# Performance work log

Hardware: AMD Instinct MI355X
Metric: run time of the kernel (lower is better)

Reference implementation:

```python
import jax, jax.numpy as jnp
import numpy as np
import math

EMBED_DIM = 2048
NUM_HEADS = 32
NUM_KV_HEADS = 8
HEAD_DIM = EMBED_DIM // NUM_HEADS  # 64
N_REP = NUM_HEADS // NUM_KV_HEADS  # 4
BATCH = 2
SEQ = 2048


def _rope_tables(seq_len, head_dim):
    # standard RoPE tables matching rotate_half convention (frequencies tiled twice)
    inv_freq = 1.0 / (10000.0 ** (np.arange(0, head_dim, 2, dtype=np.float32) / head_dim))
    t = np.arange(seq_len, dtype=np.float32)
    freqs = np.outer(t, inv_freq)                      # (seq, head_dim/2)
    emb = np.concatenate([freqs, freqs], axis=-1)      # (seq, head_dim)
    return jnp.asarray(np.cos(emb)), jnp.asarray(np.sin(emb))


def setup_inputs() -> dict:
    key = jax.random.key(0)
    ks = jax.random.split(key, 6)
    scale = 1.0 / math.sqrt(EMBED_DIM)
    x = jax.random.normal(ks[0], (BATCH, SEQ, EMBED_DIM), dtype=jnp.float32)
    wq = jax.random.normal(ks[1], (EMBED_DIM, EMBED_DIM), dtype=jnp.float32) * scale
    wk = jax.random.normal(ks[2], (NUM_KV_HEADS * HEAD_DIM, EMBED_DIM), dtype=jnp.float32) * scale
    wv = jax.random.normal(ks[3], (NUM_KV_HEADS * HEAD_DIM, EMBED_DIM), dtype=jnp.float32) * scale
    wo = jax.random.normal(ks[4], (EMBED_DIM, EMBED_DIM), dtype=jnp.float32) * scale
    freqs_cos, freqs_sin = _rope_tables(SEQ, HEAD_DIM)
    return {"x": x, "freqs_cos": freqs_cos, "freqs_sin": freqs_sin,
            "wq": wq, "wk": wk, "wv": wv, "wo": wo}


def _rotate_half(t):
    h = t.shape[-1] // 2
    return jnp.concatenate([-t[..., h:], t[..., :h]], axis=-1)


def reference(x, freqs_cos, freqs_sin, wq, wk, wv, wo):
    b, s, _ = x.shape
    # QKV projections (Linear with weight (out,in): y = x @ W^T)
    xq = (x @ wq.T).reshape(b, s, NUM_HEADS, HEAD_DIM).transpose(0, 2, 1, 3)     # (b,H,s,d)
    xk = (x @ wk.T).reshape(b, s, NUM_KV_HEADS, HEAD_DIM).transpose(0, 2, 1, 3)  # (b,Hkv,s,d)
    xv = (x @ wv.T).reshape(b, s, NUM_KV_HEADS, HEAD_DIM).transpose(0, 2, 1, 3)
    # RoPE: cos/sin (s,d) broadcast over (b,h,s,d)
    xq = xq * freqs_cos + _rotate_half(xq) * freqs_sin
    xk = xk * freqs_cos + _rotate_half(xk) * freqs_sin
    # GQA: repeat_interleave kv heads to match q heads
    xk = jnp.repeat(xk, N_REP, axis=1)  # (b,H,s,d)
    xv = jnp.repeat(xv, N_REP, axis=1)
    scores = jnp.einsum('bhqd,bhkd->bhqk', xq, xk) / math.sqrt(HEAD_DIM)
    causal = jnp.tril(jnp.ones((s, s), dtype=bool))
    scores = jnp.where(causal, scores, jnp.float32(-1e30))
    attn = jax.nn.softmax(scores, axis=-1)
    out = jnp.einsum('bhqk,bhkd->bhqd', attn, xv)        # (b,H,s,d)
    out = out.transpose(0, 2, 1, 3).reshape(b, s, EMBED_DIM)
    return out @ wo.T
```

## Files before the change

### kernel.cpp

```cpp
#include <hip/hip_runtime.h>

#define BATCH 2
#define SEQ 2048
#define EMBED 2048
#define NHEADS 32
#define NKV 8
#define HDIM 64
#define QKV_LD 3072
#define LOG2E 1.44269504088896f

typedef __attribute__((ext_vector_type(8))) short short8;
typedef __attribute__((ext_vector_type(4))) float f32x4;

__device__ inline float hw_exp2(float x) { return __builtin_amdgcn_exp2f(x); }

__device__ inline ushort f2bf(float f) {
  union { float f; unsigned u; } v{f};
  unsigned r = v.u + 0x7FFF + ((v.u >> 16) & 1);
  return (ushort)(r >> 16);
}
__device__ inline float bf2f(ushort u) {
  union { unsigned u; float f; } v{((unsigned)u) << 16};
  return v.f;
}
__device__ inline unsigned fbits(float f) {
  union { float f; unsigned u; } v{f};
  return v.u;
}

__device__ inline void gload16(const ushort* g, ushort* l) {
  __builtin_amdgcn_global_load_lds(
      (const __attribute__((address_space(1))) unsigned*)g,
      (__attribute__((address_space(3))) unsigned*)l, 16, 0, 0);
}

#define PHASE_BAR()                          \
  do {                                       \
    __builtin_amdgcn_sched_barrier(0);       \
    __builtin_amdgcn_s_barrier();            \
    __builtin_amdgcn_sched_barrier(0);       \
  } while (0)

__global__ __launch_bounds__(256) void cvt_all(const float* __restrict__ x,
                                               const float* __restrict__ wq,
                                               const float* __restrict__ wk,
                                               const float* __restrict__ wv,
                                               const float* __restrict__ wo,
                                               ushort* __restrict__ xb,
                                               ushort* __restrict__ wqkv,
                                               ushort* __restrict__ wob) {
  size_t e = (size_t)(blockIdx.x * blockDim.x + threadIdx.x) * 8;
  const float* src;
  ushort* dst;
  if (e < 8388608u) { src = x + e; dst = xb + e; }
  else if (e < 12582912u) { size_t o = e - 8388608u; src = wq + o; dst = wqkv + o; }
  else if (e < 13631488u) { size_t o = e - 12582912u; src = wk + o; dst = wqkv + 4194304u + o; }
  else if (e < 14680064u) { size_t o = e - 13631488u; src = wv + o; dst = wqkv + 5242880u + o; }
  else { size_t o = e - 14680064u; src = wo + o; dst = wob + o; }
  float4 v0 = ((const float4*)src)[0];
  float4 v1 = ((const float4*)src)[1];
  union { uint4 v; ushort u[8]; } pk;
  pk.u[0] = f2bf(v0.x); pk.u[1] = f2bf(v0.y); pk.u[2] = f2bf(v0.z); pk.u[3] = f2bf(v0.w);
  pk.u[4] = f2bf(v1.x); pk.u[5] = f2bf(v1.y); pk.u[6] = f2bf(v1.z); pk.u[7] = f2bf(v1.w);
  *(uint4*)dst = pk.v;
}

template <int BN, int MODE, typename OutT>
__global__ __launch_bounds__(512) void gemm8p(const ushort* __restrict__ Ag,
                                              const ushort* __restrict__ Bg,
                                              OutT* __restrict__ C,
                                              const float* __restrict__ fc,
                                              const float* __restrict__ fs,
                                              int M, int N, int K) {
  constexpr int NF = BN / 64;
  __shared__ ushort As[2][2][256][32];
  __shared__ ushort Bs[2][2][BN][32];
  const int tid = threadIdx.x;
  const int lane = tid & 63, wave = tid >> 6;
  const int quad = lane >> 4, l16 = lane & 15;
  const int wm = wave >> 2, wn = wave & 3;
  const int m0 = blockIdx.y * 256, n0 = blockIdx.x * BN;
  const int NT = K >> 6;

  auto stA = [&](int Tn, int h) {
    const int r0 = h * 128 + wave * 16;
    const int lrow = r0 + (lane >> 2);
    const int sw = ((lane & 3) ^ ((lrow >> 1) & 3)) * 8;
    const ushort* g = Ag + (size_t)(m0 + lrow) * K + Tn * 64 + sw;
    gload16(g, &As[Tn & 1][0][r0][0]);
    gload16(g + 32, &As[Tn & 1][1][r0][0]);
  };
  auto stB = [&](int Tn, int h) {
    const int r0 = h * 128 + wave * 16;
    const int lrow = r0 + (lane >> 2);
    const int sw = ((lane & 3) ^ ((lrow >> 1) & 3)) * 8;
    const ushort* g = Bg + (size_t)(n0 + lrow) * K + Tn * 64 + sw;
    gload16(g, &Bs[Tn & 1][0][r0][0]);
    gload16(g + 32, &Bs[Tn & 1][1][r0][0]);
  };

  f32x4 acc[8][NF] = {};

  stA(0, 0); stA(0, 1);
  stB(0, 0);
  if constexpr (BN == 256) stB(0, 1);

  for (int T = 0; T < NT; ++T) {
    const int bf = T & 1;
    asm volatile("s_waitcnt vmcnt(0)" ::: "memory");
    PHASE_BAR();

    short8 bfr[NF][2];
#pragma unroll
    for (int nf = 0; nf < NF; nf++) {
      const int row = wn * (16 * NF) + nf * 16 + l16;
      const int ch = (quad ^ ((row >> 1) & 3)) * 8;
#pragma unroll
      for (int kk = 0; kk < 2; kk++)
        bfr[nf][kk] = *(short8*)&Bs[bf][kk][row][ch];
    }

#pragma unroll
    for (int q = 0; q < 4; q++) {
      short8 afr[2][2];
#pragma unroll
      for (int mq = 0; mq < 2; mq++) {
        const int row = wm * 128 + (2 * q + mq) * 16 + l16;
        const int ch = (quad ^ ((row >> 1) & 3)) * 8;
#pragma unroll
        for (int kk = 0; kk < 2; kk++)
          afr[mq][kk] = *(short8*)&As[bf][kk][row][ch];
      }

      if (T + 1 < NT) {
        if (q == 0) stA(T + 1, 0);
        else if (q == 1) stA(T + 1, 1);
        else if (q == 2) stB(T + 1, 0);
        else if constexpr (BN == 256) stB(T + 1, 1);
      }

      __builtin_amdgcn_s_setprio(1);
#pragma unroll
      for (int mq = 0; mq < 2; mq++)
#pragma unroll
        for (int nf = 0; nf < NF; nf++)
#pragma unroll
          for (int kk = 0; kk < 2; kk++)
            acc[2 * q + mq][nf] = __builtin_amdgcn_mfma_f32_16x16x32_bf16(
                afr[mq][kk], bfr[nf][kk], acc[2 * q + mq][nf], 0, 0, 0);
      __builtin_amdgcn_s_setprio(0);
      PHASE_BAR();
    }
  }

  if constexpr (MODE == 1) {
    if (n0 < 2560) {
      const float scale = (n0 < 2048) ? 0.125f * LOG2E : 1.0f;
      const int d0 = l16, d1 = l16 + 32;
      const int e0 = l16 + 16, e1 = l16 + 48;
#pragma unroll
      for (int mf = 0; mf < 8; mf++) {
#pragma unroll
        for (int r = 0; r < 4; r++) {
          size_t rg = (size_t)(m0 + wm * 128 + mf * 16 + quad * 4 + r);
          int s = (int)(rg & (SEQ - 1));
          const float* cb = fc + s * HDIM;
          const float* sb = fs + s * HDIM;
          float x0 = acc[mf][0][r], x2 = acc[mf][2][r];
          float y1 = acc[mf][1][r], y3 = acc[mf][3][r];
          float o0 = (x0 * cb[d0] - x2 * sb[d0]) * scale;
          float o2 = (x2 * cb[d1] + x0 * sb[d1]) * scale;
          float o1 = (y1 * cb[e0] - y3 * sb[e0]) * scale;
          float o3 = (y3 * cb[e1] + y1 * sb[e1]) * scale;
          ushort* Cr = (ushort*)C + rg * N + n0 + wn * 64 + l16;
          Cr[0]  = f2bf(o0);
          Cr[16] = f2bf(o1);
          Cr[32] = f2bf(o2);
          Cr[48] = f2bf(o3);
        }
      }
      return;
    }
  }
#pragma unroll
  for (int mf = 0; mf < 8; mf++) {
#pragma unroll
    for (int r = 0; r < 4; r++) {
      size_t rg = (size_t)(m0 + wm * 128 + mf * 16 + quad * 4 + r);
#pragma unroll
      for (int nf = 0; nf < NF; nf++) {
        int cg = n0 + wn * (16 * NF) + nf * 16 + l16;
        if constexpr (sizeof(OutT) == 2)
          C[rg * N + cg] = f2bf(acc[mf][nf][r]);
        else
          C[rg * N + cg] = acc[mf][nf][r];
      }
    }
  }
}

__global__ __launch_bounds__(256, 4) void attn_mfma(const ushort* __restrict__ QKV,
                                                    ushort* __restrict__ O) {
  __shared__ ushort Ks[64][72];
  __shared__ ushort Vt[64][72];
  __shared__ ushort Pw[4][16][72];
  const int tid = threadIdx.x;
  const int lane = tid & 63, wave = tid >> 6;
  const int quad = lane >> 4, l16 = lane & 15;

  const int bid = blockIdx.x;
  const int qq = bid >> 8;
  const int j4 = (bid >> 6) & 3;
  const int bh = bid & 63;
  const int qblk = (qq >> 1) * 8 + ((qq & 1) ? 7 - j4 : j4);

  const int b = bh >> 5, h = bh & 31, kh = h >> 2;
  const int ntiles = 2 * qblk + 2;
  const int wrow = qblk * 128 + wave * 32;

  short8 qf[2][2];
#pragma unroll
  for (int f = 0; f < 2; f++)
#pragma unroll
    for (int c = 0; c < 2; c++)
      qf[f][c] = *(const short8*)(QKV +
          (size_t)(b * SEQ + wrow + f * 16 + l16) * QKV_LD +
          h * HDIM + c * 32 + quad * 8);

  f32x4 o[2][4] = {};
  float m[2] = {-INFINITY, -INFINITY}, l[2] = {0.f, 0.f};

  const ushort* Kbase = QKV + (size_t)b * SEQ * QKV_LD + 2048 + kh * HDIM;
  const ushort* Vbase = Kbase + 512;
  const int kp = tid & 31, dg = tid >> 5;

  for (int t = 0; t < ntiles; t++) {
    const int k0 = t * 64;
    __syncthreads();
    {
      const float4* kpp = (const float4*)(Kbase + (size_t)(k0 + lane) * QKV_LD + wave * 16);
      float4 kv0 = kpp[0], kv1 = kpp[1];
      const uint4* va4 = (const uint4*)(Vbase + (size_t)(k0 + 2 * kp) * QKV_LD + dg * 8);
      const uint4* vb4 = (const uint4*)(Vbase + (size_t)(k0 + 2 * kp + 1) * QKV_LD + dg * 8);
      uint4 va = va4[0], vb = vb4[0];
      *(float4*)&Ks[lane][wave * 16] = kv0;
      *(float4*)&Ks[lane][wave * 16 + 8] = kv1;
      const unsigned* vaw = (const unsigned*)&va;
      const unsigned* vbw = (const unsigned*)&vb;
#pragma unroll
      for (int j = 0; j < 8; j++) {
        unsigned pk = (j & 1)
            ? __builtin_amdgcn_perm(vbw[j >> 1], vaw[j >> 1], 0x07060302)
            : __builtin_amdgcn_perm(vbw[j >> 1], vaw[j >> 1], 0x05040100);
        *(unsigned*)&Vt[dg * 8 + j][2 * kp] = pk;
      }
    }
    __syncthreads();

    if (k0 > wrow + 31) continue;
    const bool a0 = (k0 <= wrow + 15);

    f32x4 s0[4], s1[4];
    __builtin_amdgcn_s_setprio(1);
#pragma unroll
    for (int nt = 0; nt < 4; nt++) {
      short8 kf0 = *(short8*)&Ks[nt * 16 + l16][quad * 8];
      short8 kf1 = *(short8*)&Ks[nt * 16 + l16][32 + quad * 8];
      f32x4 z1 = {};
      z1 = __builtin_amdgcn_mfma_f32_16x16x32_bf16(kf0, qf[1][0], z1, 0, 0, 0);
      s1[nt] = __builtin_amdgcn_mfma_f32_16x16x32_bf16(kf1, qf[1][1], z1, 0, 0, 0);
      if (a0) {
        f32x4 z0 = {};
        z0 = __builtin_amdgcn_mfma_f32_16x16x32_bf16(kf0, qf[0][0], z0, 0, 0, 0);
        s0[nt] = __builtin_amdgcn_mfma_f32_16x16x32_bf16(kf1, qf[0][1], z0, 0, 0, 0);
      }
    }
    __builtin_amdgcn_s_setprio(0);

    if (k0 + 63 > wrow + 16) {
      const int lim1 = wrow + 16 + l16 - k0;
#pragma unroll
      for (int nt = 0; nt < 4; nt++)
#pragma unroll
        for (int r = 0; r < 4; r++)
          if (nt * 16 + quad * 4 + r > lim1) s1[nt][r] = -INFINITY;
    }
    if (a0 && k0 + 63 > wrow) {
      const int lim0 = wrow + l16 - k0;
#pragma unroll
      for (int nt = 0; nt < 4; nt++)
#pragma unroll
        for (int r = 0; r < 4; r++)
          if (nt * 16 + quad * 4 + r > lim0) s0[nt][r] = -INFINITY;
    }

    auto smx = [&](f32x4 (&s)[4], float& mm, float& ll, f32x4 (&oo)[4]) {
      float mx = s[0][0];
#pragma unroll
      for (int nt = 0; nt < 4; nt++)
#pragma unroll
        for (int r = 0; r < 4; r++) mx = fmaxf(mx, s[nt][r]);
      if (!__all(mx <= mm + 8.f)) {
        mx = fmaxf(mx, __shfl_xor(mx, 16));
        mx = fmaxf(mx, __shfl_xor(mx, 32));
        float mnew = fmaxf(mm, mx);
        float al = hw_exp2(mm - mnew);
        mm = mnew;
        ll *= al;
#pragma unroll
        for (int dt = 0; dt < 4; dt++)
#pragma unroll
          for (int r = 0; r < 4; r++) oo[dt][r] *= al;
      }
      float psum = 0.f;
#pragma unroll
      for (int nt = 0; nt < 4; nt++) {
        float p0 = hw_exp2(s[nt][0] - mm), p1 = hw_exp2(s[nt][1] - mm);
        float p2 = hw_exp2(s[nt][2] - mm), p3 = hw_exp2(s[nt][3] - mm);
        psum += (p0 + p1) + (p2 + p3);
        unsigned lo = __builtin_amdgcn_perm(fbits(p1), fbits(p0), 0x07060302);
        unsigned hi = __builtin_amdgcn_perm(fbits(p3), fbits(p2), 0x07060302);
        uint2 pk; pk.x = lo; pk.y = hi;
        *(uint2*)&Pw[wave][l16][nt * 16 + quad * 4] = pk;
      }
      ll += psum;
    };

    short8 pf00, pf01, pf10, pf11;
    if (a0) {
      smx(s0, m[0], l[0], o[0]);
      pf00 = *(short8*)&Pw[wave][l16][quad * 8];
      pf01 = *(short8*)&Pw[wave][l16][32 + quad * 8];
    }
    smx(s1, m[1], l[1], o[1]);
    pf10 = *(short8*)&Pw[wave][l16][quad * 8];
    pf11 = *(short8*)&Pw[wave][l16][32 + quad * 8];

    __builtin_amdgcn_s_setprio(1);
#pragma unroll
    for (int dt = 0; dt < 4; dt++) {
      short8 vf0 = *(short8*)&Vt[dt * 16 + l16][quad * 8];
      short8 vf1 = *(short8*)&Vt[dt * 16 + l16][32 + quad * 8];
      o[1][dt] = __builtin_amdgcn_mfma_f32_16x16x32_bf16(vf0, pf10, o[1][dt], 0, 0, 0);
      o[1][dt] = __builtin_amdgcn_mfma_f32_16x16x32_bf16(vf1, pf11, o[1][dt], 0, 0, 0);
      if (a0) {
        o[0][dt] = __builtin_amdgcn_mfma_f32_16x16x32_bf16(vf0, pf00, o[0][dt], 0, 0, 0);
        o[0][dt] = __builtin_amdgcn_mfma_f32_16x16x32_bf16(vf1, pf01, o[0][dt], 0, 0, 0);
      }
    }
    __builtin_amdgcn_s_setprio(0);
  }

#pragma unroll
  for (int f = 0; f < 2; f++) {
    float lr = l[f];
    lr += __shfl_xor(lr, 16);
    lr += __shfl_xor(lr, 32);
    float inv = 1.0f / lr;
    size_t rowg = (size_t)(b * SEQ + wrow + f * 16 + l16) * EMBED + h * HDIM;
#pragma unroll
    for (int dt = 0; dt < 4; dt++) {
      ushort q0 = f2bf(o[f][dt][0] * inv), q1 = f2bf(o[f][dt][1] * inv);
      ushort q2 = f2bf(o[f][dt][2] * inv), q3 = f2bf(o[f][dt][3] * inv);
      uint2 pk;
      pk.x = (unsigned)q0 | ((unsigned)q1 << 16);
      pk.y = (unsigned)q2 | ((unsigned)q3 << 16);
      *(uint2*)&O[rowg + dt * 16 + quad * 4] = pk;
    }
  }
}

extern "C" void kernel_launch(void* const* d_in, const int* in_sizes, int n_in,
                              void* d_out, int out_size, void* d_ws, size_t ws_size,
                              hipStream_t stream) {
  const float* x = (const float*)d_in[0];
  const float* fcos = (const float*)d_in[1];
  const float* fsin = (const float*)d_in[2];
  const float* wq = (const float*)d_in[3];
  const float* wk = (const float*)d_in[4];
  const float* wv = (const float*)d_in[5];
  const float* wo = (const float*)d_in[6];
  float* out = (float*)d_out;

  const int M = BATCH * SEQ;
  ushort* ws = (ushort*)d_ws;
  ushort* xb = ws;
  ushort* wqkv = xb + (size_t)M * EMBED;
  ushort* wob = wqkv + (size_t)QKV_LD * EMBED;
  ushort* QKVb = wob + (size_t)EMBED * EMBED;
  ushort* Ab = QKVb + (size_t)M * QKV_LD;

  dim3 blk(256);
  cvt_all<<<9216, blk, 0, stream>>>(x, wq, wk, wv, wo, xb, wqkv, wob);

  gemm8p<256, 1, ushort><<<dim3(QKV_LD / 256, M / 256), dim3(512), 0, stream>>>(
      xb, wqkv, QKVb, fcos, fsin, M, QKV_LD, EMBED);

  attn_mfma<<<dim3(1024), blk, 0, stream>>>(QKVb, Ab);

  gemm8p<128, 0, float><<<dim3(EMBED / 128, M / 256), dim3(512), 0, stream>>>(
      Ab, wob, out, nullptr, nullptr, M, EMBED, EMBED);
}
```

Measured before the change: 304.8 us.

## Restructure GEMM into triple-buffered K=32 pipeline with partial vmcnt waits

Replaces the double-buffered K=64 GEMM, which waited on all loads and used five barriers per tile, with a three-stage LDS ring of K=32 tiles. Loads are issued two tiles ahead, and the loop waits only for the oldest tile's loads via a partial vmcnt count, with one barrier per iteration. This is meant to hide global-to-LDS latency and cut barrier overhead. In exchange, each barrier covers less MFMA work per tile, and correctness now depends on the hard-coded vmcnt counts matching the number of loads issued per stage.

```diff
diff --git a/kernel.cpp b/kernel.cpp
--- a/kernel.cpp
+++ b/kernel.cpp
@@ -33,13 +33,6 @@
       (const __attribute__((address_space(1))) unsigned*)g,
       (__attribute__((address_space(3))) unsigned*)l, 16, 0, 0);
 }
-
-#define PHASE_BAR()                          \
-  do {                                       \
-    __builtin_amdgcn_sched_barrier(0);       \
-    __builtin_amdgcn_s_barrier();            \
-    __builtin_amdgcn_sched_barrier(0);       \
-  } while (0)
 
 __global__ __launch_bounds__(256) void cvt_all(const float* __restrict__ x,
                                                const float* __restrict__ wq,
@@ -66,91 +59,93 @@
 }
 
 template <int BN, int MODE, typename OutT>
-__global__ __launch_bounds__(512) void gemm8p(const ushort* __restrict__ Ag,
+__global__ __launch_bounds__(512) void gemm3b(const ushort* __restrict__ Ag,
                                               const ushort* __restrict__ Bg,
                                               OutT* __restrict__ C,
                                               const float* __restrict__ fc,
                                               const float* __restrict__ fs,
                                               int M, int N, int K) {
   constexpr int NF = BN / 64;
-  __shared__ ushort As[2][2][256][32];
-  __shared__ ushort Bs[2][2][BN][32];
+  __shared__ ushort As[3][256][32];
+  __shared__ ushort Bs[3][BN][32];
   const int tid = threadIdx.x;
   const int lane = tid & 63, wave = tid >> 6;
   const int quad = lane >> 4, l16 = lane & 15;
   const int wm = wave >> 2, wn = wave & 3;
   const int m0 = blockIdx.y * 256, n0 = blockIdx.x * BN;
-  const int NT = K >> 6;
-
-  auto stA = [&](int Tn, int h) {
-    const int r0 = h * 128 + wave * 16;
-    const int lrow = r0 + (lane >> 2);
-    const int sw = ((lane & 3) ^ ((lrow >> 1) & 3)) * 8;
-    const ushort* g = Ag + (size_t)(m0 + lrow) * K + Tn * 64 + sw;
-    gload16(g, &As[Tn & 1][0][r0][0]);
-    gload16(g + 32, &As[Tn & 1][1][r0][0]);
+  const int NT = K >> 5;
+
+  auto stage = [&](int Tn) {
+    const int b3 = Tn % 3;
+    {
+      const int r0 = wave * 32;
+      const int lr0 = r0 + (lane >> 2);
+      const int sw0 = ((lane & 3) ^ ((lr0 >> 1) & 3)) * 8;
+      gload16(Ag + (size_t)(m0 + lr0) * K + Tn * 32 + sw0, &As[b3][r0][0]);
+      const int lr1 = lr0 + 16;
+      const int sw1 = ((lane & 3) ^ ((lr1 >> 1) & 3)) * 8;
+      gload16(Ag + (size_t)(m0 + lr1) * K + Tn * 32 + sw1, &As[b3][r0 + 16][0]);
+    }
+    if constexpr (BN == 256) {
+      const int r0 = wave * 32;
+      const int lr0 = r0 + (lane >> 2);
+      const int sw0 = ((lane & 3) ^ ((lr0 >> 1) & 3)) * 8;
+      gload16(Bg + (size_t)(n0 + lr0) * K + Tn * 32 + sw0, &Bs[b3][r0][0]);
+      const int lr1 = lr0 + 16;
+      const int sw1 = ((lane & 3) ^ ((lr1 >> 1) & 3)) * 8;
+      gload16(Bg + (size_t)(n0 + lr1) * K + Tn * 32 + sw1, &Bs[b3][r0 + 16][0]);
+    } else {
+      const int r0 = wave * 16;
+      const int lr0 = r0 + (lane >> 2);
+      const int sw0 = ((lane & 3) ^ ((lr0 >> 1) & 3)) * 8;
+      gload16(Bg + (size_t)(n0 + lr0) * K + Tn * 32 + sw0, &Bs[b3][r0][0]);
+    }
   };
-  auto stB = [&](int Tn, int h) {
-    const int r0 = h * 128 + wave * 16;
-    const int lrow = r0 + (lane >> 2);
-    const int sw = ((lane & 3) ^ ((lrow >> 1) & 3)) * 8;
-    const ushort* g = Bg + (size_t)(n0 + lrow) * K + Tn * 64 + sw;
-    gload16(g, &Bs[Tn & 1][0][r0][0]);
-    gload16(g + 32, &Bs[Tn & 1][1][r0][0]);
-  };
 
   f32x4 acc[8][NF] = {};
 
-  stA(0, 0); stA(0, 1);
-  stB(0, 0);
-  if constexpr (BN == 256) stB(0, 1);
+  stage(0);
+  stage(1);
 
   for (int T = 0; T < NT; ++T) {
-    const int bf = T & 1;
-    asm volatile("s_waitcnt vmcnt(0)" ::: "memory");
-    PHASE_BAR();
-
-    short8 bfr[NF][2];
+    const int b3 = T % 3;
+    if (T + 1 < NT) {
+      if constexpr (BN == 256)
+        asm volatile("s_waitcnt vmcnt(4)" ::: "memory");
+      else
+        asm volatile("s_waitcnt vmcnt(3)" ::: "memory");
+    } else {
+      asm volatile("s_waitcnt vmcnt(0)" ::: "memory");
+    }
+    __builtin_amdgcn_sched_barrier(0);
+    __builtin_amdgcn_s_barrier();
+    __builtin_amdgcn_sched_barrier(0);
+
+    if (T + 2 < NT) stage(T + 2);
+
+    short8 bfr[NF];
 #pragma unroll
     for (int nf = 0; nf < NF; nf++) {
       const int row = wn * (16 * NF) + nf * 16 + l16;
       const int ch = (quad ^ ((row >> 1) & 3)) * 8;
-#pragma unroll
-      for (int kk = 0; kk < 2; kk++)
-        bfr[nf][kk] = *(short8*)&Bs[bf][kk][row][ch];
-    }
-
-#pragma unroll
-    for (int q = 0; q < 4; q++) {
-      short8 afr[2][2];
-#pragma unroll
-      for (int mq = 0; mq < 2; mq++) {
-        const int row = wm * 128 + (2 * q + mq) * 16 + l16;
-        const int ch = (quad ^ ((row >> 1) & 3)) * 8;
-#pragma unroll
-        for (int kk = 0; kk < 2; kk++)
-          afr[mq][kk] = *(short8*)&As[bf][kk][row][ch];
-      }
-
-      if (T + 1 < NT) {
-        if (q == 0) stA(T + 1, 0);
-        else if (q == 1) stA(T + 1, 1);
-        else if (q == 2) stB(T + 1, 0);
-        else if constexpr (BN == 256) stB(T + 1, 1);
-      }
-
-      __builtin_amdgcn_s_setprio(1);
-#pragma unroll
-      for (int mq = 0; mq < 2; mq++)
-#pragma unroll
-        for (int nf = 0; nf < NF; nf++)
-#pragma unroll
-          for (int kk = 0; kk < 2; kk++)
-            acc[2 * q + mq][nf] = __builtin_amdgcn_mfma_f32_16x16x32_bf16(
-                afr[mq][kk], bfr[nf][kk], acc[2 * q + mq][nf], 0, 0, 0);
-      __builtin_amdgcn_s_setprio(0);
-      PHASE_BAR();
-    }
+      bfr[nf] = *(short8*)&Bs[b3][row][ch];
+    }
+    short8 afr[8];
+#pragma unroll
+    for (int mf = 0; mf < 8; mf++) {
+      const int row = wm * 128 + mf * 16 + l16;
+      const int ch = (quad ^ ((row >> 1) & 3)) * 8;
+      afr[mf] = *(short8*)&As[b3][row][ch];
+    }
+
+    __builtin_amdgcn_s_setprio(1);
+#pragma unroll
+    for (int mf = 0; mf < 8; mf++)
+#pragma unroll
+      for (int nf = 0; nf < NF; nf++)
+        acc[mf][nf] = __builtin_amdgcn_mfma_f32_16x16x32_bf16(
+            afr[mf], bfr[nf], acc[mf][nf], 0, 0, 0);
+    __builtin_amdgcn_s_setprio(0);
   }
 
   if constexpr (MODE == 1) {
@@ -393,11 +388,11 @@
   dim3 blk(256);
   cvt_all<<<9216, blk, 0, stream>>>(x, wq, wk, wv, wo, xb, wqkv, wob);
 
-  gemm8p<256, 1, ushort><<<dim3(QKV_LD / 256, M / 256), dim3(512), 0, stream>>>(
+  gemm3b<256, 1, ushort><<<dim3(QKV_LD / 256, M / 256), dim3(512), 0, stream>>>(
       xb, wqkv, QKVb, fcos, fsin, M, QKV_LD, EMBED);
 
   attn_mfma<<<dim3(1024), blk, 0, stream>>>(QKVb, Ab);
 
-  gemm8p<128, 0, float><<<dim3(EMBED / 128, M / 256), dim3(512), 0, stream>>>(
+  gemm3b<128, 0, float><<<dim3(EMBED / 128, M / 256), dim3(512), 0, stream>>>(
       Ab, wob, out, nullptr, nullptr, M, EMBED, EMBED);
 }
```

After: 338.1 us. 10.9% more time.
